# Optimization experiments

Hardware: AMD Instinct MI355X
Metric: run time of the kernel (lower is better)

## Reference

```python
import jax, jax.numpy as jnp
import numpy as np

T, H = 8192, 512
MC, MD = 4096, 4096
N_ENT = 128
MAX_DIST = 600  # POSITION_EMBEDDING_IN_DIM


def _make_spans(k, m, t):
    ks, kl = jax.random.split(k)
    starts = jax.random.randint(ks, (m,), 0, t - 8, dtype=jnp.int64)
    lens = jax.random.randint(kl, (m,), 0, 8, dtype=jnp.int64)
    return jnp.stack([starts, starts + lens], axis=1)  # inclusive [start, end], end < T


def setup_inputs() -> dict:
    key = jax.random.key(0)
    k = jax.random.split(key, 8)
    h = jax.random.normal(k[0], (T, H), dtype=jnp.float32)
    chem_spans = _make_spans(k[1], MC, T)
    dis_spans = _make_spans(k[2], MD, T)
    # deterministic entity assignment guarantees every entity has mentions
    chem_ent = jnp.arange(MC, dtype=jnp.int64) % N_ENT
    dis_ent = jnp.arange(MD, dtype=jnp.int64) % N_ENT
    s = 0.05
    return {
        "h": h,
        "chem_spans": chem_spans, "chem_ent": chem_ent,
        "dis_spans": dis_spans, "dis_ent": dis_ent,
        "Wc": jax.random.normal(k[3], (H, 100), jnp.float32) * s,
        "bc": jnp.zeros((100,), jnp.float32),
        "Wd": jax.random.normal(k[4], (H, 100), jnp.float32) * s,
        "bd": jnp.zeros((100,), jnp.float32),
        "Wemb": jax.random.normal(k[5], (MAX_DIST, 50), jnp.float32),
        "Ws": jax.random.normal(k[6], (250, 2), jnp.float32) * s,
        "bs": jnp.zeros((2,), jnp.float32),
        "n_chem": N_ENT,
        "n_dis": N_ENT,
    }


def reference(h, chem_spans, chem_ent, dis_spans, dis_ent,
              Wc, bc, Wd, bd, Wemb, Ws, bs, n_chem, n_dis):
    # inclusive span sums via prefix sums: sum(h[s..e]) = csum[e+1] - csum[s]
    csum = jnp.concatenate([jnp.zeros((1, h.shape[1]), h.dtype), jnp.cumsum(h, axis=0)], axis=0)
    c_sum = csum[chem_spans[:, 1] + 1] - csum[chem_spans[:, 0]]  # [MC, H]
    d_sum = csum[dis_spans[:, 1] + 1] - csum[dis_spans[:, 0]]    # [MD, H]
    c_feat = jnp.tanh(c_sum @ Wc + bc)  # [MC, 100]
    d_feat = jnp.tanh(d_sum @ Wd + bd)  # [MD, 100]
    # score Dense over concat(c, d, emb) decomposed linearly (same math)
    sc_c = c_feat @ Ws[:100]            # [MC, 2]
    sc_d = d_feat @ Ws[100:200]         # [MD, 2]
    emb_sc = Wemb @ Ws[200:250]         # [600, 2] pre-contracted embedding scores
    dist = jnp.minimum(jnp.abs(chem_spans[:, 0][:, None] - dis_spans[:, 0][None, :]),
                       MAX_DIST - 1)    # [MC, MD]
    pair = sc_c[:, None, :] + sc_d[None, :, :] + emb_sc[dist] + bs  # [MC, MD, 2]
    # running max over all mention pairs of each (chem entity, disease entity)
    pair_ids = (chem_ent[:, None] * n_dis + dis_ent[None, :]).reshape(-1)
    neg = jnp.full((n_chem * n_dis, 2), -jnp.inf, dtype=pair.dtype)
    ent_max = neg.at[pair_ids].max(pair.reshape(-1, 2))
    return jax.nn.softmax(ent_max, axis=-1).reshape(n_chem, n_dis, 2)
```

## Files before the change

kernel.cpp:

```cpp
#include <hip/hip_runtime.h>
#include <math.h>
#include <limits.h>

#define H_DIM  512
#define NFEAT  100
#define NPAD   112
#define NT     7
#define KW     4
#define MAXD   600
#define MAXE   2048
#define SB     16
#define CHK    64
#define DCH    64

#define NEG_ENC 0x007FFFFFu

typedef __attribute__((ext_vector_type(8))) short short8v;
typedef __attribute__((ext_vector_type(4))) float f32x4;

__device__ __forceinline__ unsigned enc_f(float f){
    unsigned u = __float_as_uint(f);
    return (u & 0x80000000u) ? ~u : (u | 0x80000000u);
}
__device__ __forceinline__ float dec_f(unsigned e){
    unsigned u = (e & 0x80000000u) ? (e ^ 0x80000000u) : ~e;
    return __uint_as_float(u);
}
__device__ __forceinline__ unsigned short f2bf(float f){
    unsigned x = __float_as_uint(f);
    return (unsigned short)((x + 0x7fffu + ((x >> 16) & 1u)) >> 16);
}

__global__ __launch_bounds__(256) void prep_kernel(
    const float* __restrict__ h,
    const float* __restrict__ Wemb, const float* __restrict__ Ws,
    const float* __restrict__ bs,
    const float* __restrict__ Wc,   const float* __restrict__ Wd,
    const int* __restrict__ cent, const int* __restrict__ dent,
    const int* __restrict__ ncp,  const int* __restrict__ ndp,
    const int* __restrict__ cspans, const int* __restrict__ dspans,
    float* __restrict__ emb2, unsigned* __restrict__ gent, int gent_n,
    unsigned short* __restrict__ Wt, unsigned short* __restrict__ S,
    int* __restrict__ ghist,
    int MCv, int MDv, int MCs16, int Rtot, int off_e, int off_w, int off_h)
{
    const int tid = threadIdx.x;
    const int bid = blockIdx.x;

    if (bid < 32){
        __shared__ int hist[MAXE];
        const int side = bid >> 4;
        const int b    = bid & 15;
        const int ne   = side ? *ndp : *ncp;
        if (ne > MAXE) return;
        const int* ent = side ? dent : cent;
        const int  M   = side ? MDv : MCv;
        const int chunk = (M + SB - 1) / SB;
        const int i0 = b * chunk, i1 = min(M, i0 + chunk);
        for (int e = tid; e < ne; e += 256) hist[e] = 0;
        __syncthreads();
        for (int i = i0 + tid; i < i1; i += 256) atomicAdd(&hist[ent[i]], 1);
        __syncthreads();
        int* gh = ghist + (side*SB + b) * MAXE;
        for (int e = tid; e < ne; e += 256) gh[e] = hist[e];
    } else if (bid < off_e){
        int i = (bid - 32) * 256 + tid;
        if (i < gent_n) gent[i] = NEG_ENC;
    } else if (bid < off_w){
        int d = (bid - off_e) * 256 + tid;
        if (d < MAXD){
            float a0 = bs[0], a1 = bs[1];
            #pragma unroll 5
            for (int q = 0; q < 50; ++q){
                float w = Wemb[d*50 + q];
                a0 += w * Ws[(200+q)*2 + 0];
                a1 += w * Ws[(200+q)*2 + 1];
            }
            emb2[d*2 + 0] = a0;
            emb2[d*2 + 1] = a1;
        }
    } else if (bid < off_h){
        const int base = (bid - off_w) * 4096;
        #pragma unroll
        for (int ii = 0; ii < 16; ++ii){
            int e = base + tid + 256*ii;
            if (e < 2*NPAD*H_DIM){
                int side = e / (NPAD*H_DIM);
                int rem  = e - side*(NPAD*H_DIM);
                int n    = rem / H_DIM;
                int k    = rem - n*H_DIM;
                const float* W = side ? Wd : Wc;
                Wt[e] = (n < NFEAT) ? f2bf(W[k*NFEAT + n]) : (unsigned short)0;
            }
        }
    } else {
        const int row = (bid - off_h) * 4 + (tid >> 6);
        if (row < Rtot){
            const int side = (row >= MCs16);
            const int ml   = side ? (row - MCs16) : row;
            const int M    = side ? MDv : MCv;
            const int col0 = (tid & 63) * 8;
            float a0=0.f,a1=0.f,a2=0.f,a3=0.f,a4=0.f,a5=0.f,a6=0.f,a7=0.f;
            if (ml < M){
                const int* spans = side ? dspans : cspans;
                const int s   = spans[ml*2];
                const int len = spans[ml*2 + 1] - s;
                const float* hp = h + (size_t)s * H_DIM + col0;
                float4 v0[8], v1[8];
                #pragma unroll
                for (int r = 0; r < 8; ++r){
                    v0[r] = *reinterpret_cast<const float4*>(hp + (size_t)r*H_DIM);
                    v1[r] = *reinterpret_cast<const float4*>(hp + (size_t)r*H_DIM + 4);
                }
                #pragma unroll
                for (int r = 0; r < 8; ++r){
                    if (r <= len){
                        a0+=v0[r].x; a1+=v0[r].y; a2+=v0[r].z; a3+=v0[r].w;
                        a4+=v1[r].x; a5+=v1[r].y; a6+=v1[r].z; a7+=v1[r].w;
                    }
                }
            }
            union { unsigned short us[8]; uint4 v; } o;
            o.us[0]=f2bf(a0); o.us[1]=f2bf(a1); o.us[2]=f2bf(a2); o.us[3]=f2bf(a3);
            o.us[4]=f2bf(a4); o.us[5]=f2bf(a5); o.us[6]=f2bf(a6); o.us[7]=f2bf(a7);
            *reinterpret_cast<uint4*>(S + (size_t)row * H_DIM + col0) = o.v;
        }
    }
}

__global__ __launch_bounds__(256) void gemm_feat(
    const unsigned short* __restrict__ S,
    const unsigned short* __restrict__ Wt,
    const float* __restrict__ bc, const float* __restrict__ bd,
    const float* __restrict__ Ws,
    float* __restrict__ sc_c, float* __restrict__ sc_d,
    const int* __restrict__ cent, const int* __restrict__ dent,
    const int* __restrict__ ncp,  const int* __restrict__ ndp,
    const int* __restrict__ cspans, const int* __restrict__ dspans,
    const int* __restrict__ ghist,
    int4* __restrict__ csorted, int4* __restrict__ dsorted,
    int mtc, int mtd, int MCv, int MDv, int MCs16)
{
    __shared__ float s_acc[KW-1][NT*4][64];
    __shared__ int   s_tot[MAXE];
    __shared__ int   s_cur[MAXE];
    __shared__ int   s_wsum[4];

    const int tid  = threadIdx.x;
    const int lane = tid & 63;
    const int w    = tid >> 6;
    const int bid  = blockIdx.x;

    if (bid >= mtc + mtd){
        const int sb   = bid - (mtc + mtd);
        const int side = sb >> 4;
        const int b    = sb & 15;
        const int ne   = side ? *ndp : *ncp;
        const int* ent = side ? dent : cent;
        const int* spans = side ? dspans : cspans;
        int4* out      = side ? dsorted : csorted;
        const int M    = side ? MDv : MCv;
        const int chunk = (M + SB - 1) / SB;
        const int i0 = b * chunk, i1 = min(M, i0 + chunk);

        if (ne <= MAXE){
            const int* gh = ghist + side*SB*MAXE;
            for (int e = tid; e < ne; e += 256){
                int pre = 0, tot = 0;
                #pragma unroll
                for (int bb = 0; bb < SB; ++bb){
                    int v = gh[bb*MAXE + e];
                    tot += v;
                    pre += (bb < b) ? v : 0;
                }
                s_tot[e] = tot;
                s_cur[e] = pre;
            }
            __syncthreads();
            const int per = (ne + 255) / 256;
            const int lo = min(tid*per, ne), hi = min(lo + per, ne);
            int sum = 0;
            for (int j = lo; j < hi; ++j) sum += s_tot[j];
            int x = sum;
            #pragma unroll
            for (int k = 1; k < 64; k <<= 1){
                int y = __shfl_up(x, k);
                if (lane >= k) x += y;
            }
            int excl = x - sum;
            if (lane == 63) s_wsum[w] = x;
            __syncthreads();
            for (int ww = 0; ww < w; ++ww) excl += s_wsum[ww];
            int run = excl;
            for (int j = lo; j < hi; ++j){
                s_cur[j] += run;
                run += s_tot[j];
            }
            __syncthreads();
            for (int i = i0 + tid; i < i1; i += 256){
                int e = ent[i];
                int pos = atomicAdd(&s_cur[e], 1);
                out[pos] = make_int4(spans[i*2], e, i, 0);
            }
        } else {
            for (int i = i0 + tid; i < i1; i += 256)
                out[i] = make_int4(spans[i*2], ent[i], i, 0);
        }
        return;
    }

    const int side = (bid >= mtc);
    const int mt   = side ? (bid - mtc) : bid;
    const int row0 = (side ? MCs16 : 0) + mt*16;

    const unsigned short* A = S + (size_t)(row0 + (lane & 15)) * H_DIM
                                + (lane >> 4) * 8 + w * 4 * 32;
    const unsigned short* B = Wt + (size_t)side * NPAD * H_DIM
                                 + (size_t)(lane & 15) * H_DIM
                                 + (lane >> 4) * 8 + w * 4 * 32;

    f32x4 acc[NT];
    #pragma unroll
    for (int nt = 0; nt < NT; ++nt) acc[nt] = (f32x4){0.f,0.f,0.f,0.f};

    #pragma unroll
    for (int ks = 0; ks < 4; ++ks){
        short8v a = *reinterpret_cast<const short8v*>(A + ks*32);
        #pragma unroll
        for (int nt = 0; nt < NT; ++nt){
            short8v b = *reinterpret_cast<const short8v*>(B + (size_t)nt*16*H_DIM + ks*32);
            acc[nt] = __builtin_amdgcn_mfma_f32_16x16x32_bf16(a, b, acc[nt], 0, 0, 0);
        }
    }

    if (w > 0){
        #pragma unroll
        for (int nt = 0; nt < NT; ++nt)
            #pragma unroll
            for (int r = 0; r < 4; ++r)
                s_acc[w-1][nt*4 + r][lane] = acc[nt][r];
    }
    __syncthreads();
    if (w == 0){
        #pragma unroll
        for (int nt = 0; nt < NT; ++nt)
            #pragma unroll
            for (int r = 0; r < 4; ++r)
                acc[nt][r] += s_acc[0][nt*4+r][lane]
                            + s_acc[1][nt*4+r][lane]
                            + s_acc[2][nt*4+r][lane];

        const float* bvec = side ? bd : bc;
        const int    wsoff = side ? NFEAT : 0;
        const int    nb    = lane & 15;
        float bb[NT], w0[NT], w1[NT];
        #pragma unroll
        for (int nt = 0; nt < NT; ++nt){
            int n = nt*16 + nb;
            bool v = (n < NFEAT);
            bb[nt] = v ? bvec[n] : 0.f;
            w0[nt] = v ? Ws[(wsoff + n)*2 + 0] : 0.f;
            w1[nt] = v ? Ws[(wsoff + n)*2 + 1] : 0.f;
        }
        const int ml0 = mt*16 + (lane >> 4)*4;
        const int M   = side ? MDv : MCv;
        float* sc     = side ? sc_d : sc_c;
        #pragma unroll
        for (int r = 0; r < 4; ++r){
            float p0 = 0.f, p1 = 0.f;
            #pragma unroll
            for (int nt = 0; nt < NT; ++nt){
                float f = tanhf(acc[nt][r] + bb[nt]);
                p0 += f * w0[nt];
                p1 += f * w1[nt];
            }
            #pragma unroll
            for (int k = 1; k < 16; k <<= 1){
                p0 += __shfl_xor(p0, k);
                p1 += __shfl_xor(p1, k);
            }
            int ml = ml0 + r;
            if (nb == 0 && ml < M){
                sc[ml*2 + 0] = p0;
                sc[ml*2 + 1] = p1;
            }
        }
    }
}

__device__ __forceinline__ void flush_run(
    float s0, float s1, int ce, int de, int nd, bool head,
    const bool okk[6], unsigned* __restrict__ gent)
{
    float a0 = s0, a1 = s1;
    #pragma unroll
    for (int k = 0; k < 6; ++k){
        float b0 = __shfl_down(a0, 1 << k);
        float b1 = __shfl_down(a1, 1 << k);
        if (okk[k]){ a0 = fmaxf(a0, b0); a1 = fmaxf(a1, b1); }
    }
    if (head && ce != INT_MAX){
        atomicMax(&gent[(ce*nd + de)*2 + 0], enc_f(a0));
        atomicMax(&gent[(ce*nd + de)*2 + 1], enc_f(a1));
    }
}

__global__ __launch_bounds__(256) void pair_kernel(
    const int4* __restrict__ csorted, const int4* __restrict__ dsorted,
    const float* __restrict__ sc_c,   const float* __restrict__ sc_d,
    const float* __restrict__ emb2,   const int* __restrict__ ndp,
    unsigned* __restrict__ gent, int MCv, int MDv)
{
    __shared__ float2 s_e[MAXD];
    __shared__ int4   s_d[CHK];

    const int tid  = threadIdx.x;
    const int lane = tid & 63;
    const int nd   = *ndp;

    const float2* e2 = (const float2*)emb2;
    for (int i = tid; i < MAXD; i += 256) s_e[i] = e2[i];

    int   cs = 0, ce = INT_MAX;
    float c0 = 0.f, c1 = 0.f;
    {
        int ci = blockIdx.x * 256 + tid;
        if (ci < MCv){
            int4 r = csorted[ci];
            cs = r.x; ce = r.y;
            const float2 sc = *reinterpret_cast<const float2*>(&sc_c[2*r.z]);
            c0 = sc.x; c1 = sc.y;
        }
    }
    int ceprev = __shfl_up(ce, 1);
    const bool head = (lane == 0) || (ceprev != ce);
    bool okk[6];
    #pragma unroll
    for (int k = 0; k < 6; ++k) okk[k] = (__shfl_down(ce, 1 << k) == ce);

    for (int cb = blockIdx.y; cb * CHK < MDv; cb += DCH){
        const int dbase = cb * CHK;
        const int n = min(CHK, MDv - dbase);
        __syncthreads();
        for (int i = tid; i < n; i += 256){
            int4 r = dsorted[dbase + i];
            const float2 sd = *reinterpret_cast<const float2*>(&sc_d[2*r.z]);
            s_d[i] = make_int4(r.x, r.y, __float_as_int(sd.x), __float_as_int(sd.y));
        }
        __syncthreads();

        int   cur_de = s_d[0].y;
        float s0 = -INFINITY, s1 = -INFINITY;
        for (int j = 0; j < n; ++j){
            int4 dj = s_d[j];
            if (dj.y != cur_de){
                flush_run(s0, s1, ce, cur_de, nd, head, okk, gent);
                cur_de = dj.y; s0 = -INFINITY; s1 = -INFINITY;
            }
            int dd = cs - dj.x; dd = dd < 0 ? -dd : dd;
            dd = dd < (MAXD-1) ? dd : (MAXD-1);
            float2 e = s_e[dd];
            s0 = fmaxf(s0, c0 + __int_as_float(dj.z) + e.x);
            s1 = fmaxf(s1, c1 + __int_as_float(dj.w) + e.y);
        }
        flush_run(s0, s1, ce, cur_de, nd, head, okk, gent);
    }
}

__global__ void softmax_kernel(const unsigned* __restrict__ gent,
                               float* __restrict__ out, int npairs){
    int p = blockIdx.x * blockDim.x + threadIdx.x;
    if (p < npairs){
        float a = dec_f(gent[p*2 + 0]);
        float b = dec_f(gent[p*2 + 1]);
        float m = fmaxf(a, b);
        float ea = expf(a - m), eb = expf(b - m);
        float inv = 1.f / (ea + eb);
        out[p*2 + 0] = ea * inv;
        out[p*2 + 1] = eb * inv;
    }
}

extern "C" void kernel_launch(void* const* d_in, const int* in_sizes, int n_in,
                              void* d_out, int out_size, void* d_ws, size_t ws_size,
                              hipStream_t stream)
{
    const float* h      = (const float*)d_in[0];
    const int*   cspans = (const int*)  d_in[1];
    const int*   centp  = (const int*)  d_in[2];
    const int*   dspans = (const int*)  d_in[3];
    const int*   dentp  = (const int*)  d_in[4];
    const float* Wc     = (const float*)d_in[5];
    const float* bc     = (const float*)d_in[6];
    const float* Wd     = (const float*)d_in[7];
    const float* bd     = (const float*)d_in[8];
    const float* Wemb   = (const float*)d_in[9];
    const float* Ws     = (const float*)d_in[10];
    const float* bs     = (const float*)d_in[11];
    const int*   ncp    = (const int*)  d_in[12];
    const int*   ndp    = (const int*)  d_in[13];

    const int MCv    = in_sizes[1] / 2;
    const int MDv    = in_sizes[3] / 2;
    const int npairs = out_size / 2;

    const int mtc   = (MCv + 15) / 16;
    const int mtd   = (MDv + 15) / 16;
    const int MCs16 = mtc * 16;
    const int Rtot  = (mtc + mtd) * 16;

    float*    wsf    = (float*)d_ws;
    float*    emb2   = wsf;
    float*    sc_c   = wsf + 1280;
    float*    sc_d   = sc_c + (size_t)MCv * 2;
    unsigned* gent   = (unsigned*)(sc_d + (size_t)MDv * 2);
    int4*     csorted= (int4*)(gent + out_size);
    int4*     dsorted= csorted + MCv;
    unsigned short* S  = (unsigned short*)(dsorted + MDv);
    unsigned short* Wt = S + (size_t)Rtot * H_DIM;
    int*      ghist  = (int*)(Wt + 2 * NPAD * H_DIM);

    const int gb    = (out_size + 255) / 256;
    const int eb    = (MAXD + 255) / 256;
    const int wb    = (2*NPAD*H_DIM + 4095) / 4096;
    const int sb    = (Rtot + 3) / 4;
    const int off_e = 32 + gb;
    const int off_w = off_e + eb;
    const int off_h = off_w + wb;

    hipLaunchKernelGGL(prep_kernel, dim3(off_h + sb), dim3(256), 0, stream,
                       h, Wemb, Ws, bs, Wc, Wd, centp, dentp, ncp, ndp,
                       cspans, dspans, emb2, gent, out_size, Wt, S, ghist,
                       MCv, MDv, MCs16, Rtot, off_e, off_w, off_h);

    hipLaunchKernelGGL(gemm_feat, dim3(mtc + mtd + 32), dim3(256), 0, stream,
                       S, Wt, bc, bd, Ws, sc_c, sc_d,
                       centp, dentp, ncp, ndp, cspans, dspans,
                       ghist, csorted, dsorted, mtc, mtd, MCv, MDv, MCs16);

    hipLaunchKernelGGL(pair_kernel, dim3((MCv + 255)/256, DCH), dim3(256), 0, stream,
                       csorted, dsorted, sc_c, sc_d, emb2, ndp, gent, MCv, MDv);

    hipLaunchKernelGGL(softmax_kernel, dim3((npairs + 255)/256), dim3(256), 0, stream,
                       gent, (float*)d_out, npairs);
}
```

Before: 131.7 us.

## Fuse span-sum into GEMM via LDS and fold softmax into pair kernel tail

Span sums of h are now computed inside gemm_feat and written as bf16 rows straight to shared memory, instead of being produced by prep_kernel and stored to a global S buffer. This removes the global write and re-read of S. The separate softmax launch is replaced by a last-block-done pattern in pair_kernel, using an atomic counter and threadfence, which removes one launch. The cost is that a single block runs the whole softmax serially over all pairs, and the shared-memory regions are now aliased.

```diff
diff --git a/kernel.cpp b/kernel.cpp
--- a/kernel.cpp
+++ b/kernel.cpp
@@ -7,6 +7,7 @@
 #define NPAD   112
 #define NT     7
 #define KW     4
+#define SROW   520
 #define MAXD   600
 #define MAXE   2048
 #define SB     16
@@ -32,17 +33,15 @@
 }
 
 __global__ __launch_bounds__(256) void prep_kernel(
-    const float* __restrict__ h,
     const float* __restrict__ Wemb, const float* __restrict__ Ws,
     const float* __restrict__ bs,
     const float* __restrict__ Wc,   const float* __restrict__ Wd,
     const int* __restrict__ cent, const int* __restrict__ dent,
     const int* __restrict__ ncp,  const int* __restrict__ ndp,
-    const int* __restrict__ cspans, const int* __restrict__ dspans,
     float* __restrict__ emb2, unsigned* __restrict__ gent, int gent_n,
-    unsigned short* __restrict__ Wt, unsigned short* __restrict__ S,
-    int* __restrict__ ghist,
-    int MCv, int MDv, int MCs16, int Rtot, int off_e, int off_w, int off_h)
+    unsigned short* __restrict__ Wt, int* __restrict__ ghist,
+    unsigned* __restrict__ cnt,
+    int MCv, int MDv, int off_e, int off_w)
 {
     const int tid = threadIdx.x;
     const int bid = blockIdx.x;
@@ -64,6 +63,7 @@
         int* gh = ghist + (side*SB + b) * MAXE;
         for (int e = tid; e < ne; e += 256) gh[e] = hist[e];
     } else if (bid < off_e){
+        if (bid == 32 && tid == 0) *cnt = 0u;
         int i = (bid - 32) * 256 + tid;
         if (i < gent_n) gent[i] = NEG_ENC;
     } else if (bid < off_w){
@@ -79,7 +79,7 @@
             emb2[d*2 + 0] = a0;
             emb2[d*2 + 1] = a1;
         }
-    } else if (bid < off_h){
+    } else {
         const int base = (bid - off_w) * 4096;
         #pragma unroll
         for (int ii = 0; ii < 16; ++ii){
@@ -93,43 +93,11 @@
                 Wt[e] = (n < NFEAT) ? f2bf(W[k*NFEAT + n]) : (unsigned short)0;
             }
         }
-    } else {
-        const int row = (bid - off_h) * 4 + (tid >> 6);
-        if (row < Rtot){
-            const int side = (row >= MCs16);
-            const int ml   = side ? (row - MCs16) : row;
-            const int M    = side ? MDv : MCv;
-            const int col0 = (tid & 63) * 8;
-            float a0=0.f,a1=0.f,a2=0.f,a3=0.f,a4=0.f,a5=0.f,a6=0.f,a7=0.f;
-            if (ml < M){
-                const int* spans = side ? dspans : cspans;
-                const int s   = spans[ml*2];
-                const int len = spans[ml*2 + 1] - s;
-                const float* hp = h + (size_t)s * H_DIM + col0;
-                float4 v0[8], v1[8];
-                #pragma unroll
-                for (int r = 0; r < 8; ++r){
-                    v0[r] = *reinterpret_cast<const float4*>(hp + (size_t)r*H_DIM);
-                    v1[r] = *reinterpret_cast<const float4*>(hp + (size_t)r*H_DIM + 4);
-                }
-                #pragma unroll
-                for (int r = 0; r < 8; ++r){
-                    if (r <= len){
-                        a0+=v0[r].x; a1+=v0[r].y; a2+=v0[r].z; a3+=v0[r].w;
-                        a4+=v1[r].x; a5+=v1[r].y; a6+=v1[r].z; a7+=v1[r].w;
-                    }
-                }
-            }
-            union { unsigned short us[8]; uint4 v; } o;
-            o.us[0]=f2bf(a0); o.us[1]=f2bf(a1); o.us[2]=f2bf(a2); o.us[3]=f2bf(a3);
-            o.us[4]=f2bf(a4); o.us[5]=f2bf(a5); o.us[6]=f2bf(a6); o.us[7]=f2bf(a7);
-            *reinterpret_cast<uint4*>(S + (size_t)row * H_DIM + col0) = o.v;
-        }
     }
 }
 
 __global__ __launch_bounds__(256) void gemm_feat(
-    const unsigned short* __restrict__ S,
+    const float* __restrict__ h,
     const unsigned short* __restrict__ Wt,
     const float* __restrict__ bc, const float* __restrict__ bd,
     const float* __restrict__ Ws,
@@ -139,12 +107,14 @@
     const int* __restrict__ cspans, const int* __restrict__ dspans,
     const int* __restrict__ ghist,
     int4* __restrict__ csorted, int4* __restrict__ dsorted,
-    int mtc, int mtd, int MCv, int MDv, int MCs16)
+    int mtc, int mtd, int MCv, int MDv)
 {
-    __shared__ float s_acc[KW-1][NT*4][64];
-    __shared__ int   s_tot[MAXE];
-    __shared__ int   s_cur[MAXE];
-    __shared__ int   s_wsum[4];
+    __shared__ __align__(16) char smem[38160];
+    unsigned short* S_lds = (unsigned short*)smem;
+    float*          s_acc = (float*)(smem + 16640);
+    int*            s_tot = (int*)smem;
+    int*            s_cur = (int*)(smem + 8192);
+    int*            s_wsum= (int*)(smem + 16384);
 
     const int tid  = threadIdx.x;
     const int lane = tid & 63;
@@ -211,13 +181,46 @@
 
     const int side = (bid >= mtc);
     const int mt   = side ? (bid - mtc) : bid;
-    const int row0 = (side ? MCs16 : 0) + mt*16;
-
-    const unsigned short* A = S + (size_t)(row0 + (lane & 15)) * H_DIM
-                                + (lane >> 4) * 8 + w * 4 * 32;
+    const int* spans = side ? dspans : cspans;
+    const int  M     = side ? MDv : MCv;
+
+    #pragma unroll
+    for (int rr = 0; rr < 4; ++rr){
+        const int rloc = w*4 + rr;
+        const int ml   = mt*16 + rloc;
+        float A0=0.f,A1=0.f,A2=0.f,A3=0.f,A4=0.f,A5=0.f,A6=0.f,A7=0.f;
+        if (ml < M){
+            const int s   = spans[ml*2];
+            const int len = spans[ml*2 + 1] - s;
+            const float* hp = h + (size_t)s * H_DIM + lane*8;
+#define RW(r) { const float4* p_ = (const float4*)(hp + (size_t)(r)*H_DIM); \
+                float4 u0=p_[0], u1=p_[1]; \
+                A0+=u0.x; A1+=u0.y; A2+=u0.z; A3+=u0.w; \
+                A4+=u1.x; A5+=u1.y; A6+=u1.z; A7+=u1.w; }
+            switch(len){
+                case 7: RW(7);
+                case 6: RW(6);
+                case 5: RW(5);
+                case 4: RW(4);
+                case 3: RW(3);
+                case 2: RW(2);
+                case 1: RW(1);
+                default: RW(0);
+            }
+#undef RW
+        }
+        union { unsigned short us[8]; uint4 v; } o;
+        o.us[0]=f2bf(A0); o.us[1]=f2bf(A1); o.us[2]=f2bf(A2); o.us[3]=f2bf(A3);
+        o.us[4]=f2bf(A4); o.us[5]=f2bf(A5); o.us[6]=f2bf(A6); o.us[7]=f2bf(A7);
+        *reinterpret_cast<uint4*>(S_lds + rloc*SROW + lane*8) = o.v;
+    }
+    __syncthreads();
+
     const unsigned short* B = Wt + (size_t)side * NPAD * H_DIM
                                  + (size_t)(lane & 15) * H_DIM
                                  + (lane >> 4) * 8 + w * 4 * 32;
+    const unsigned short* Al = S_lds + (lane & 15) * SROW
+                                     + (lane >> 4) * 8 + w * 4 * 32;
 
     f32x4 acc[NT];
     #pragma unroll
@@ -225,7 +228,7 @@
 
     #pragma unroll
     for (int ks = 0; ks < 4; ++ks){
-        short8v a = *reinterpret_cast<const short8v*>(A + ks*32);
+        short8v a = *reinterpret_cast<const short8v*>(Al + ks*32);
         #pragma unroll
         for (int nt = 0; nt < NT; ++nt){
             short8v b = *reinterpret_cast<const short8v*>(B + (size_t)nt*16*H_DIM + ks*32);
@@ -238,7 +241,7 @@
         for (int nt = 0; nt < NT; ++nt)
             #pragma unroll
             for (int r = 0; r < 4; ++r)
-                s_acc[w-1][nt*4 + r][lane] = acc[nt][r];
+                s_acc[((w-1)*28 + nt*4 + r)*64 + lane] = acc[nt][r];
     }
     __syncthreads();
     if (w == 0){
@@ -246,9 +249,9 @@
         for (int nt = 0; nt < NT; ++nt)
             #pragma unroll
             for (int r = 0; r < 4; ++r)
-                acc[nt][r] += s_acc[0][nt*4+r][lane]
-                            + s_acc[1][nt*4+r][lane]
-                            + s_acc[2][nt*4+r][lane];
+                acc[nt][r] += s_acc[(nt*4+r)*64 + lane]
+                            + s_acc[(28 + nt*4+r)*64 + lane]
+                            + s_acc[(56 + nt*4+r)*64 + lane];
 
         const float* bvec = side ? bd : bc;
         const int    wsoff = side ? NFEAT : 0;
@@ -263,7 +266,6 @@
             w1[nt] = v ? Ws[(wsoff + n)*2 + 1] : 0.f;
         }
         const int ml0 = mt*16 + (lane >> 4)*4;
-        const int M   = side ? MDv : MCv;
         float* sc     = side ? sc_d : sc_c;
         #pragma unroll
         for (int r = 0; r < 4; ++r){
@@ -309,10 +311,13 @@
     const int4* __restrict__ csorted, const int4* __restrict__ dsorted,
     const float* __restrict__ sc_c,   const float* __restrict__ sc_d,
     const float* __restrict__ emb2,   const int* __restrict__ ndp,
-    unsigned* __restrict__ gent, int MCv, int MDv)
+    unsigned* __restrict__ gent, int MCv, int MDv,
+    unsigned* __restrict__ cnt, float* __restrict__ out,
+    int npairs, int nblocks)
 {
     __shared__ float2 s_e[MAXD];
     __shared__ int4   s_d[CHK];
+    __shared__ int    s_last;
 
     const int tid  = threadIdx.x;
     const int lane = tid & 63;
@@ -365,19 +370,22 @@
         }
         flush_run(s0, s1, ce, cur_de, nd, head, okk, gent);
     }
-}
-
-__global__ void softmax_kernel(const unsigned* __restrict__ gent,
-                               float* __restrict__ out, int npairs){
-    int p = blockIdx.x * blockDim.x + threadIdx.x;
-    if (p < npairs){
-        float a = dec_f(gent[p*2 + 0]);
-        float b = dec_f(gent[p*2 + 1]);
-        float m = fmaxf(a, b);
-        float ea = expf(a - m), eb = expf(b - m);
-        float inv = 1.f / (ea + eb);
-        out[p*2 + 0] = ea * inv;
-        out[p*2 + 1] = eb * inv;
+
+    __threadfence();
+    __syncthreads();
+    if (tid == 0) s_last = (atomicAdd(cnt, 1u) == (unsigned)(nblocks - 1));
+    __syncthreads();
+    if (s_last){
+        __threadfence();
+        for (int p = tid; p < npairs; p += 256){
+            float a = dec_f(gent[p*2 + 0]);
+            float b = dec_f(gent[p*2 + 1]);
+            float m = fmaxf(a, b);
+            float ea = expf(a - m), eb = expf(b - m);
+            float inv = 1.f / (ea + eb);
+            out[p*2 + 0] = ea * inv;
+            out[p*2 + 1] = eb * inv;
+        }
     }
 }
 
@@ -404,10 +412,8 @@
     const int MDv    = in_sizes[3] / 2;
     const int npairs = out_size / 2;
 
-    const int mtc   = (MCv + 15) / 16;
-    const int mtd   = (MDv + 15) / 16;
-    const int MCs16 = mtc * 16;
-    const int Rtot  = (mtc + mtd) * 16;
+    const int mtc = (MCv + 15) / 16;
+    const int mtd = (MDv + 15) / 16;
 
     float*    wsf    = (float*)d_ws;
     float*    emb2   = wsf;
@@ -416,31 +422,28 @@
     unsigned* gent   = (unsigned*)(sc_d + (size_t)MDv * 2);
     int4*     csorted= (int4*)(gent + out_size);
     int4*     dsorted= csorted + MCv;
-    unsigned short* S  = (unsigned short*)(dsorted + MDv);
-    unsigned short* Wt = S + (size_t)Rtot * H_DIM;
+    unsigned short* Wt = (unsigned short*)(dsorted + MDv);
     int*      ghist  = (int*)(Wt + 2 * NPAD * H_DIM);
+    unsigned* cnt    = (unsigned*)(ghist + 2 * SB * MAXE);
 
     const int gb    = (out_size + 255) / 256;
     const int eb    = (MAXD + 255) / 256;
     const int wb    = (2*NPAD*H_DIM + 4095) / 4096;
-    const int sb    = (Rtot + 3) / 4;
     const int off_e = 32 + gb;
     const int off_w = off_e + eb;
-    const int off_h = off_w + wb;
-
-    hipLaunchKernelGGL(prep_kernel, dim3(off_h + sb), dim3(256), 0, stream,
-                       h, Wemb, Ws, bs, Wc, Wd, centp, dentp, ncp, ndp,
-                       cspans, dspans, emb2, gent, out_size, Wt, S, ghist,
-                       MCv, MDv, MCs16, Rtot, off_e, off_w, off_h);
+
+    hipLaunchKernelGGL(prep_kernel, dim3(off_w + wb), dim3(256), 0, stream,
+                       Wemb, Ws, bs, Wc, Wd, centp, dentp, ncp, ndp,
+                       emb2, gent, out_size, Wt, ghist, cnt,
+                       MCv, MDv, off_e, off_w);
 
     hipLaunchKernelGGL(gemm_feat, dim3(mtc + mtd + 32), dim3(256), 0, stream,
-                       S, Wt, bc, bd, Ws, sc_c, sc_d,
+                       h, Wt, bc, bd, Ws, sc_c, sc_d,
                        centp, dentp, ncp, ndp, cspans, dspans,
-                       ghist, csorted, dsorted, mtc, mtd, MCv, MDv, MCs16);
-
-    hipLaunchKernelGGL(pair_kernel, dim3((MCv + 255)/256, DCH), dim3(256), 0, stream,
-                       csorted, dsorted, sc_c, sc_d, emb2, ndp, gent, MCv, MDv);
-
-    hipLaunchKernelGGL(softmax_kernel, dim3((npairs + 255)/256), dim3(256), 0, stream,
-                       gent, (float*)d_out, npairs);
-}
+                       ghist, csorted, dsorted, mtc, mtd, MCv, MDv);
+
+    const int gx = (MCv + 255) / 256;
+    hipLaunchKernelGGL(pair_kernel, dim3(gx, DCH), dim3(256), 0, stream,
+                       csorted, dsorted, sc_c, sc_d, emb2, ndp, gent, MCv, MDv,
+                       cnt, (float*)d_out, npairs, gx * DCH);
+}
```

New measurement: 200.7 us. 1.52x slower.
